# Optimization experiments

Measured on AMD Instinct MI355X. Metric: run time of the kernel, lower is better.

Reference implementation:

```python
import jax, jax.numpy as jnp
import numpy as np

B, S, D = 4, 2048, 1024
H = 16
HD = D // H  # 64


def setup_inputs() -> dict:
    key = jax.random.key(0)
    ks = jax.random.split(key, 6)
    scale = 1.0 / np.sqrt(D)
    return {
        "x": jax.random.normal(ks[0], (B, S, D), dtype=jnp.float32),
        "W_q": jax.random.normal(ks[1], (D, D), dtype=jnp.float32) * scale,
        "W_k": jax.random.normal(ks[2], (D, D), dtype=jnp.float32) * scale,
        "W_v": jax.random.normal(ks[3], (D, D), dtype=jnp.float32) * scale,
        "W_o": jax.random.normal(ks[4], (D, D), dtype=jnp.float32) * scale,
        "b_o": jax.random.normal(ks[5], (D,), dtype=jnp.float32) * 0.01,
    }


def reference(x, W_q, W_k, W_v, W_o, b_o):
    b, n, _ = x.shape
    # projections (Linear stores weight as [out,in]; here W_* are [in,out])
    q = (x @ W_q).reshape(b, n, H, HD).transpose(0, 2, 1, 3)  # [b,h,n,hd]
    k = (x @ W_k).reshape(b, n, H, HD).transpose(0, 2, 1, 3)
    v = (x @ W_v).reshape(b, n, H, HD).transpose(0, 2, 1, 3)
    scores = jnp.einsum("bhqd,bhkd->bhqk", q, k) / np.sqrt(HD).astype(np.float32)
    causal = jnp.tril(jnp.ones((n, n), dtype=bool))  # True = keep
    scores = jnp.where(causal, scores, -jnp.inf)
    weights = jax.nn.softmax(scores, axis=-1)
    ctx = jnp.einsum("bhqk,bhkd->bhqd", weights, v)
    ctx = ctx.transpose(0, 2, 1, 3).reshape(b, n, D)
    return ctx @ W_o + b_o
```

## Files before the change

### kernel.cpp

```cpp
#include <hip/hip_runtime.h>
#include <cstdint>

#define S_LEN 2048
#define D_MODEL 1024
#define NH 16
#define HDIM 64
#define BATCH 4

typedef __attribute__((ext_vector_type(8))) __bf16 bfrag;
typedef __attribute__((ext_vector_type(4))) float ffrag;

__device__ __forceinline__ unsigned short f2bf(float f) {
    union { float f; uint32_t u; } v; v.f = f;
    uint32_t u = v.u;
    u += 0x7fff + ((u >> 16) & 1);
    return (unsigned short)(u >> 16);
}

__device__ __forceinline__ bfrag ld_frag(const unsigned short* p) {
    union { uint4 u; bfrag b; } x;
    x.u = *(const uint4*)p;
    return x.b;
}

__device__ __forceinline__ float fast_exp2(float x) {
#if __has_builtin(__builtin_amdgcn_exp2f)
    return __builtin_amdgcn_exp2f(x);
#else
    return __expf(x * 0.6931471805599453f);
#endif
}

__device__ __forceinline__ uint32_t pack_bf16(float a, float b) {
    union { float f; uint32_t u; } x, y; x.f = a; y.f = b;
    return __builtin_amdgcn_perm(y.u + 0x8000u, x.u + 0x8000u, 0x07060302u);
}

__device__ __forceinline__ void g2l16(const unsigned short* g, unsigned short* l) {
    __builtin_amdgcn_global_load_lds(
        (const __attribute__((address_space(1))) void*)g,
        (__attribute__((address_space(3))) void*)l, 16, 0, 0);
}

__global__ __launch_bounds__(256) void prep_kernel(const float* __restrict__ x,
                                                   const float* __restrict__ w0,
                                                   const float* __restrict__ w1,
                                                   const float* __restrict__ w2,
                                                   const float* __restrict__ w3,
                                                   unsigned short* __restrict__ xb,
                                                   unsigned short* __restrict__ wt) {
    __shared__ float tile[32][33];
    int bid = blockIdx.x;
    int t = threadIdx.x;
    if (bid < 4096) {
        int i = bid * 256 + t;
        const float4* p = (const float4*)x + (size_t)i * 2;
        float4 a = p[0], b = p[1];
        union { unsigned short u[8]; uint4 v; } o;
        o.u[0]=f2bf(a.x); o.u[1]=f2bf(a.y); o.u[2]=f2bf(a.z); o.u[3]=f2bf(a.w);
        o.u[4]=f2bf(b.x); o.u[5]=f2bf(b.y); o.u[6]=f2bf(b.z); o.u[7]=f2bf(b.w);
        ((uint4*)xb)[i] = o.v;
    } else {
        int r = bid - 4096;
        int mat = r >> 10;
        int rem = r & 1023;
        const float* w = (mat == 0) ? w0 : (mat == 1) ? w1 : (mat == 2) ? w2 : w3;
        int n0 = (rem & 31) * 32, k0 = (rem >> 5) * 32;
        int tx = t & 31, ty = t >> 5;
        for (int i = 0; i < 32; i += 8)
            tile[ty + i][tx] = w[(size_t)(k0 + ty + i) * D_MODEL + n0 + tx];
        __syncthreads();
        unsigned short* o = wt + (size_t)mat * D_MODEL * D_MODEL;
        for (int i = 0; i < 32; i += 8)
            o[(size_t)(n0 + ty + i) * D_MODEL + (k0 + tx)] = f2bf(tile[tx][ty + i]);
    }
}

__global__ __launch_bounds__(256) void transpose_v_kernel(const unsigned short* __restrict__ Vb,
                                                          unsigned short* __restrict__ Vtb) {
    __shared__ unsigned short tile[64][72];
    int st = blockIdx.x;
    int bh = blockIdx.y;
    int t = threadIdx.x;
    int sl = t >> 2, dc = (t & 3) * 16;
    const unsigned short* src = Vb + ((size_t)bh * S_LEN + st * 64 + sl) * HDIM + dc;
    *(uint4*)&tile[sl][dc]     = *(const uint4*)(src);
    *(uint4*)&tile[sl][dc + 8] = *(const uint4*)(src + 8);
    __syncthreads();
    int d = t >> 2, sc = (t & 3) * 16;
    union { unsigned short u[16]; uint4 v[2]; } o;
#pragma unroll
    for (int i = 0; i < 16; i++) o.u[i] = tile[sc + i][d];
    unsigned short* dst = Vtb + ((size_t)bh * HDIM + d) * S_LEN + st * 64 + sc;
    *(uint4*)(dst)     = o.v[0];
    *(uint4*)(dst + 8) = o.v[1];
}

#define GBUF 4096

__global__ __launch_bounds__(256) void gemm_kernel(
    const unsigned short* __restrict__ A,
    const unsigned short* __restrict__ Bt,
    int mode,
    unsigned short* __restrict__ Qb,
    unsigned short* __restrict__ Kb,
    unsigned short* __restrict__ Vb,
    float* __restrict__ Out,
    const float* __restrict__ bias) {
    __shared__ unsigned short As[2 * GBUF];
    __shared__ unsigned short Bs[2 * GBUF];
    int t = threadIdx.x;
    int m0 = blockIdx.y * 128;
    int n0 = blockIdx.x * 128;
    int wave = t >> 6, lane = t & 63;
    int quad = lane >> 4, lrow = lane & 15;
    int wm = (wave & 1) * 64, wn = (wave >> 1) * 64;

    ffrag acc[4][4];
    const ffrag fz = {0.f, 0.f, 0.f, 0.f};
    for (int i = 0; i < 4; i++)
        for (int j = 0; j < 4; j++) acc[i][j] = fz;

    int c0 = t, c1 = 256 + t;
    int r0 = c0 >> 2, cg0 = (c0 & 3) ^ ((r0 >> 1) & 3);
    int r1 = c1 >> 2, cg1 = (c1 & 3) ^ ((r1 >> 1) & 3);
    const unsigned short* A0 = A + (size_t)(m0 + r0) * D_MODEL + cg0 * 8;
    const unsigned short* A1 = A + (size_t)(m0 + r1) * D_MODEL + cg1 * 8;
    const unsigned short* B0 = Bt + (size_t)(n0 + r0) * D_MODEL + cg0 * 8;
    const unsigned short* B1 = Bt + (size_t)(n0 + r1) * D_MODEL + cg1 * 8;
    unsigned short* lA0 = &As[(wave * 64) * 8];
    unsigned short* lA1 = &As[(256 + wave * 64) * 8];
    unsigned short* lB0 = &Bs[(wave * 64) * 8];
    unsigned short* lB1 = &Bs[(256 + wave * 64) * 8];

    g2l16(A0, lA0);
    g2l16(A1, lA1);
    g2l16(B0, lB0);
    g2l16(B1, lB1);

    for (int k0 = 0; k0 < D_MODEL; k0 += 32) {
        int buf = ((k0 >> 5) & 1) * GBUF;
        __syncthreads();
        if (k0 + 32 < D_MODEL) {
            int nb = (((k0 >> 5) + 1) & 1) * GBUF;
            g2l16(A0 + k0 + 32, lA0 + nb);
            g2l16(A1 + k0 + 32, lA1 + nb);
            g2l16(B0 + k0 + 32, lB0 + nb);
            g2l16(B1 + k0 + 32, lB1 + nb);
        }
        bfrag af[4], bf[4];
        for (int mi = 0; mi < 4; mi++) {
            int row = wm + mi * 16 + lrow;
            af[mi] = ld_frag(&As[buf + row * 32 + ((quad ^ ((row >> 1) & 3)) * 8)]);
        }
        for (int ni = 0; ni < 4; ni++) {
            int row = wn + ni * 16 + lrow;
            bf[ni] = ld_frag(&Bs[buf + row * 32 + ((quad ^ ((row >> 1) & 3)) * 8)]);
        }
        for (int mi = 0; mi < 4; mi++)
            for (int ni = 0; ni < 4; ni++)
                acc[mi][ni] = __builtin_amdgcn_mfma_f32_16x16x32_bf16(af[mi], bf[ni], acc[mi][ni], 0, 0, 0);
    }

    for (int mi = 0; mi < 4; mi++) {
        int row = m0 + wm + mi * 16 + quad * 4;
        for (int ni = 0; ni < 4; ni++) {
            int col = n0 + wn + ni * 16 + lrow;
            for (int r = 0; r < 4; r++) {
                float v = acc[mi][ni][r];
                int m = row + r;
                if (mode == 0) {
                    int matid = col >> 10;
                    int nn = col & 1023;
                    int h = nn >> 6, d = nn & 63;
                    int b = m >> 11, s = m & 2047;
                    size_t bh = (size_t)(b * NH + h);
                    if (matid == 0)      Qb[(bh * S_LEN + s) * HDIM + d] = f2bf(v);
                    else if (matid == 1) Kb[(bh * S_LEN + s) * HDIM + d] = f2bf(v);
                    else                 Vb[(bh * S_LEN + s) * HDIM + d] = f2bf(v);
                } else {
                    Out[(size_t)m * D_MODEL + col] = v + bias[col];
                }
            }
        }
    }
}

#define SCALE2 0.18033688f
#define CSHIFT 4.0f
#define KVBUF 4096

__global__ __launch_bounds__(256, 4) void attn_kernel(
    const unsigned short* __restrict__ Qb,
    const unsigned short* __restrict__ Kb,
    const unsigned short* __restrict__ Vtb,
    unsigned short* __restrict__ ctxb) {
    __shared__ unsigned short Ks[2 * KVBUF];
    __shared__ unsigned short Vs[2 * KVBUF];
    __shared__ unsigned short Ps[4 * 16 * 64];
    int bx = blockIdx.x;
    int bh = blockIdx.y;
    int t = threadIdx.x;
    int wave = t >> 6, lane = t & 63;
    int quad = lane >> 4, lrow = lane & 15;
    int swz = lrow & 7;
    int ca = (quad ^ swz) * 8;
    int cb = ca ^ 32;

    union { uint4 u; bfrag b; } one_u;
    one_u.u.x = 0x3F803F80u; one_u.u.y = 0x3F803F80u;
    one_u.u.z = 0x3F803F80u; one_u.u.w = 0x3F803F80u;
    bfrag onef = one_u.b;

    const unsigned short* Qg = Qb + (size_t)bh * S_LEN * HDIM;
    const unsigned short* Kg = Kb + (size_t)bh * S_LEN * HDIM;
    const unsigned short* Vg = Vtb + (size_t)bh * HDIM * S_LEN;
    int b = bh >> 4, h = bh & 15;

    int c0 = t, c1 = 256 + t;
    int kr0 = c0 >> 3, kp0 = (c0 & 7) ^ (kr0 & 7);
    int kr1 = c1 >> 3, kp1 = (c1 & 7) ^ (kr1 & 7);
    const unsigned short* pK0 = Kg + (size_t)kr0 * HDIM + kp0 * 8;
    const unsigned short* pK1 = Kg + (size_t)kr1 * HDIM + kp1 * 8;
    const unsigned short* pV0 = Vg + (size_t)kr0 * S_LEN + kp0 * 8;
    const unsigned short* pV1 = Vg + (size_t)kr1 * S_LEN + kp1 * 8;
    unsigned short* lK0 = &Ks[(wave * 64) * 8];
    unsigned short* lK1 = &Ks[(256 + wave * 64) * 8];
    unsigned short* lV0 = &Vs[(wave * 64) * 8];
    unsigned short* lV1 = &Vs[(256 + wave * 64) * 8];
    unsigned short* Pw = &Ps[wave * 16 * 64];

    for (int ph = 0; ph < 2; ph++) {
        int qc = ph == 0 ? (31 - bx) : bx;
        int qw = qc * 64 + wave * 16;
        int nk = qc + 1;

        bfrag qf[2];
#pragma unroll
        for (int c = 0; c < 2; c++)
            qf[c] = ld_frag(Qg + (size_t)(qw + lrow) * HDIM + c * 32 + quad * 8);

        ffrag acc[4];
        ffrag acc_l;
        const ffrag fz = {0.f, 0.f, 0.f, 0.f};
#pragma unroll
        for (int d = 0; d < 4; d++) acc[d] = fz;
        acc_l = fz;

        __syncthreads();
        g2l16(pK0, lK0);
        g2l16(pK1, lK1);
        g2l16(pV0, lV0);
        g2l16(pV1, lV1);

        for (int kt = 0; kt < nk; kt++) {
            int kbase = kt * 64;
            int buf = (kt & 1) * KVBUF;
            __syncthreads();
            if (kt + 1 < nk) {
                int nb = ((kt + 1) & 1) * KVBUF;
                size_t krow_off = (size_t)(kbase + 64) * HDIM;
                g2l16(pK0 + krow_off, lK0 + nb);
                g2l16(pK1 + krow_off, lK1 + nb);
                g2l16(pV0 + kbase + 64, lV0 + nb);
                g2l16(pV1 + kbase + 64, lV1 + nb);
            }

            ffrag sf[4];
#pragma unroll
            for (int ki = 0; ki < 4; ki++) {
                int krow = buf + (ki * 16 + lrow) * 64;
                bfrag ka = ld_frag(&Ks[krow + ca]);
                bfrag kb = ld_frag(&Ks[krow + cb]);
                ffrag s = fz;
                s = __builtin_amdgcn_mfma_f32_16x16x32_bf16(ka, qf[0], s, 0, 0, 0);
                s = __builtin_amdgcn_mfma_f32_16x16x32_bf16(kb, qf[1], s, 0, 0, 0);
                sf[ki] = s;
            }

            int qg = qw + lrow;
            bool need_mask = (kt == nk - 1);
            float sv[16];
#pragma unroll
            for (int ki = 0; ki < 4; ki++)
#pragma unroll
                for (int r = 0; r < 4; r++) {
                    float v = sf[ki][r];
                    if (need_mask) {
                        int key = kbase + ki * 16 + quad * 4 + r;
                        v = (key <= qg) ? v : -3.0e38f;
                    }
                    sv[ki * 4 + r] = fast_exp2(__builtin_fmaf(v, SCALE2, -CSHIFT));
                }
            int prow = lrow * 64;
#pragma unroll
            for (int ki = 0; ki < 4; ki++) {
                uint2 w2;
                w2.x = pack_bf16(sv[ki * 4 + 0], sv[ki * 4 + 1]);
                w2.y = pack_bf16(sv[ki * 4 + 2], sv[ki * 4 + 3]);
                int pc = ((ki * 2 + (quad >> 1)) ^ swz) * 8 + (quad & 1) * 4;
                *(uint2*)&Pw[prow + pc] = w2;
            }

            bfrag pf0 = ld_frag(&Pw[prow + ca]);
            bfrag pf1 = ld_frag(&Pw[prow + cb]);
            acc_l = __builtin_amdgcn_mfma_f32_16x16x32_bf16(onef, pf0, acc_l, 0, 0, 0);
            acc_l = __builtin_amdgcn_mfma_f32_16x16x32_bf16(onef, pf1, acc_l, 0, 0, 0);
#pragma unroll
            for (int di = 0; di < 4; di++) {
                int vrow = buf + (di * 16 + lrow) * 64;
                bfrag va = ld_frag(&Vs[vrow + ca]);
                bfrag vb = ld_frag(&Vs[vrow + cb]);
                acc[di] = __builtin_amdgcn_mfma_f32_16x16x32_bf16(va, pf0, acc[di], 0, 0, 0);
                acc[di] = __builtin_amdgcn_mfma_f32_16x16x32_bf16(vb, pf1, acc[di], 0, 0, 0);
            }
        }

        float rl = __builtin_amdgcn_rcpf(acc_l[0]);
#pragma unroll
        for (int di = 0; di < 4; di++) {
            uint2 w2;
            w2.x = pack_bf16(acc[di][0] * rl, acc[di][1] * rl);
            w2.y = pack_bf16(acc[di][2] * rl, acc[di][3] * rl);
            *(uint2*)&Pw[lrow * 64 + di * 16 + quad * 4] = w2;
        }
        int ql = lane >> 3, cc = lane & 7;
#pragma unroll
        for (int p = 0; p < 2; p++) {
            uint4 vv = *(uint4*)&Pw[(p * 8 + ql) * 64 + cc * 8];
            int q = qw + p * 8 + ql;
            *(uint4*)(ctxb + ((size_t)b * S_LEN + q) * D_MODEL + h * HDIM + cc * 8) = vv;
        }
    }
}

extern "C" void kernel_launch(void* const* d_in, const int* in_sizes, int n_in,
                              void* d_out, int out_size, void* d_ws, size_t ws_size,
                              hipStream_t stream) {
    const float* x   = (const float*)d_in[0];
    const float* W_q = (const float*)d_in[1];
    const float* W_k = (const float*)d_in[2];
    const float* W_v = (const float*)d_in[3];
    const float* W_o = (const float*)d_in[4];
    const float* b_o = (const float*)d_in[5];
    float* out = (float*)d_out;

    unsigned short* xb   = (unsigned short*)d_ws;
    unsigned short* Wt   = xb + (size_t)8192 * 1024;
    unsigned short* Qb   = Wt + (size_t)4 * 1024 * 1024;
    unsigned short* Kb   = Qb + (size_t)64 * 2048 * 64;
    unsigned short* Vtb  = Kb + (size_t)64 * 2048 * 64;
    unsigned short* ctxb = Vtb + (size_t)64 * 2048 * 64;
    unsigned short* Vb   = ctxb;
    unsigned short* Wto  = Wt + (size_t)3 * 1024 * 1024;

    prep_kernel<<<8192, 256, 0, stream>>>(x, W_q, W_k, W_v, W_o, xb, Wt);
    gemm_kernel<<<dim3(24, 64), 256, 0, stream>>>(xb, Wt, 0, Qb, Kb, Vb, nullptr, nullptr);
    transpose_v_kernel<<<dim3(32, 64), 256, 0, stream>>>(Vb, Vtb);
    attn_kernel<<<dim3(16, 64), 256, 0, stream>>>(Qb, Kb, Vtb, ctxb);
    gemm_kernel<<<dim3(8, 64), 256, 0, stream>>>(ctxb, Wto, 1, nullptr, nullptr, nullptr, out, b_o);
}
```

Before: 283.4 us.

## Triple-buffer GEMM LDS pipeline and remap workgroups across XCDs

The GEMM main loop moves from double-buffered to triple-buffered LDS, with tiles prefetched two steps ahead. Each step waits on a partial vmcnt plus a barrier, so a global-to-LDS load can stay in flight while the MFMAs run. Both the GEMM and attention kernels also remap flat block IDs so that consecutive logical tiles land on the same XCD (8-way interleave), aiming for better L2 locality. The cost is 50% more LDS in the GEMM, which may reduce occupancy. The attention remap hardcodes a grid of 1024 blocks (16x64).

```diff
diff --git a/kernel.cpp b/kernel.cpp
--- a/kernel.cpp
+++ b/kernel.cpp
@@ -97,6 +97,7 @@
 }
 
 #define GBUF 4096
+#define NKT  (D_MODEL / 32)
 
 __global__ __launch_bounds__(256) void gemm_kernel(
     const unsigned short* __restrict__ A,
@@ -107,11 +108,17 @@
     unsigned short* __restrict__ Vb,
     float* __restrict__ Out,
     const float* __restrict__ bias) {
-    __shared__ unsigned short As[2 * GBUF];
-    __shared__ unsigned short Bs[2 * GBUF];
+    __shared__ unsigned short As[3 * GBUF];
+    __shared__ unsigned short Bs[3 * GBUF];
     int t = threadIdx.x;
-    int m0 = blockIdx.y * 128;
-    int n0 = blockIdx.x * 128;
+
+    int nwg  = (int)(gridDim.x * gridDim.y);
+    int flat = (int)(blockIdx.y * gridDim.x + blockIdx.x);
+    int cpx  = nwg >> 3;
+    int wid  = (flat & 7) * cpx + (flat >> 3);
+    int m0 = (wid / (int)gridDim.x) * 128;
+    int n0 = (wid % (int)gridDim.x) * 128;
+
     int wave = t >> 6, lane = t & 63;
     int quad = lane >> 4, lrow = lane & 15;
     int wm = (wave & 1) * 64, wn = (wave >> 1) * 64;
@@ -137,25 +144,48 @@
     g2l16(A1, lA1);
     g2l16(B0, lB0);
     g2l16(B1, lB1);
-
-    for (int k0 = 0; k0 < D_MODEL; k0 += 32) {
-        int buf = ((k0 >> 5) & 1) * GBUF;
-        __syncthreads();
-        if (k0 + 32 < D_MODEL) {
-            int nb = (((k0 >> 5) + 1) & 1) * GBUF;
-            g2l16(A0 + k0 + 32, lA0 + nb);
-            g2l16(A1 + k0 + 32, lA1 + nb);
-            g2l16(B0 + k0 + 32, lB0 + nb);
-            g2l16(B1 + k0 + 32, lB1 + nb);
+    g2l16(A0 + 32, lA0 + GBUF);
+    g2l16(A1 + 32, lA1 + GBUF);
+    g2l16(B0 + 32, lB0 + GBUF);
+    g2l16(B1 + 32, lB1 + GBUF);
+
+    int bufA = 0, bufB = GBUF, bufC = 2 * GBUF;
+
+    for (int kt = 0; kt < NKT - 1; ++kt) {
+        asm volatile("s_waitcnt vmcnt(4)\n\ts_barrier" ::: "memory");
+        __builtin_amdgcn_sched_barrier(0);
+        if (kt + 2 < NKT) {
+            int ko = (kt + 2) * 32;
+            g2l16(A0 + ko, lA0 + bufC);
+            g2l16(A1 + ko, lA1 + bufC);
+            g2l16(B0 + ko, lB0 + bufC);
+            g2l16(B1 + ko, lB1 + bufC);
         }
         bfrag af[4], bf[4];
         for (int mi = 0; mi < 4; mi++) {
             int row = wm + mi * 16 + lrow;
-            af[mi] = ld_frag(&As[buf + row * 32 + ((quad ^ ((row >> 1) & 3)) * 8)]);
+            af[mi] = ld_frag(&As[bufA + row * 32 + ((quad ^ ((row >> 1) & 3)) * 8)]);
         }
         for (int ni = 0; ni < 4; ni++) {
             int row = wn + ni * 16 + lrow;
-            bf[ni] = ld_frag(&Bs[buf + row * 32 + ((quad ^ ((row >> 1) & 3)) * 8)]);
+            bf[ni] = ld_frag(&Bs[bufA + row * 32 + ((quad ^ ((row >> 1) & 3)) * 8)]);
+        }
+        for (int mi = 0; mi < 4; mi++)
+            for (int ni = 0; ni < 4; ni++)
+                acc[mi][ni] = __builtin_amdgcn_mfma_f32_16x16x32_bf16(af[mi], bf[ni], acc[mi][ni], 0, 0, 0);
+        int tmp = bufA; bufA = bufB; bufB = bufC; bufC = tmp;
+    }
+    asm volatile("s_waitcnt vmcnt(0)\n\ts_barrier" ::: "memory");
+    __builtin_amdgcn_sched_barrier(0);
+    {
+        bfrag af[4], bf[4];
+        for (int mi = 0; mi < 4; mi++) {
+            int row = wm + mi * 16 + lrow;
+            af[mi] = ld_frag(&As[bufA + row * 32 + ((quad ^ ((row >> 1) & 3)) * 8)]);
+        }
+        for (int ni = 0; ni < 4; ni++) {
+            int row = wn + ni * 16 + lrow;
+            bf[ni] = ld_frag(&Bs[bufA + row * 32 + ((quad ^ ((row >> 1) & 3)) * 8)]);
         }
         for (int mi = 0; mi < 4; mi++)
             for (int ni = 0; ni < 4; ni++)
@@ -198,8 +228,10 @@
     __shared__ unsigned short Ks[2 * KVBUF];
     __shared__ unsigned short Vs[2 * KVBUF];
     __shared__ unsigned short Ps[4 * 16 * 64];
-    int bx = blockIdx.x;
-    int bh = blockIdx.y;
+    int flat = (int)(blockIdx.y * gridDim.x + blockIdx.x);
+    int wid  = (flat & 7) * 128 + (flat >> 3);
+    int bx = wid & 15;
+    int bh = wid >> 4;
     int t = threadIdx.x;
     int wave = t >> 6, lane = t & 63;
     int quad = lane >> 4, lrow = lane & 15;
```

New measurement: 281.1 us. About the same (-0.8%).
